# Optimization experiments

Measured on AMD Instinct MI355X. Metric: run time of the kernel, lower is better.

The kernel has to match this reference:

```python
import jax, jax.numpy as jnp
import numpy as np

NUM_HEADS = 16
EPS = 1e-5
CHUNK = 128  # chunk length for the chunked recurrent-state scan


def _linear_attention(x, Wq, Wk, Wv, Wo, bo):
    B, T, E = x.shape
    H = NUM_HEADS
    d = E // H

    def proj(W):
        # nn.Linear(bias=False): y = x @ W.T ; split heads -> (B,H,T,d)
        return (x @ W.T).reshape(B, T, H, d).transpose(0, 2, 1, 3)

    phi_q = jax.nn.elu(proj(Wq)) + 1.0
    phi_k = jax.nn.elu(proj(Wk)) + 1.0
    V = proj(Wv)

    nC = T // CHUNK
    # (nC, B, H, C, d) so lax.scan iterates over chunks of time
    def to_chunks(a):
        return a.reshape(B, H, nC, CHUNK, d).transpose(2, 0, 1, 3, 4)

    qc, kc, vc = to_chunks(phi_q), to_chunks(phi_k), to_chunks(V)
    mask = jnp.tril(jnp.ones((CHUNK, CHUNK), x.dtype))  # causal incl. diagonal

    S0 = jnp.zeros((B, H, d, d), x.dtype)  # running sum of k v^T
    z0 = jnp.zeros((B, H, d), x.dtype)     # running sum of phi_k

    def step(carry, inp):
        S, z = carry
        q, k, v = inp  # (B,H,C,d)
        A = jnp.einsum('bhid,bhjd->bhij', q, k) * mask
        num = jnp.einsum('bhij,bhjd->bhid', A, v) + jnp.einsum('bhid,bhde->bhie', q, S)
        den = jnp.sum(A, axis=-1) + jnp.einsum('bhid,bhd->bhi', q, z) + EPS
        out = num / den[..., None]
        S = S + jnp.einsum('bhjd,bhje->bhde', k, v)
        z = z + jnp.sum(k, axis=2)
        return (S, z), out

    _, outs = jax.lax.scan(step, (S0, z0), (qc, kc, vc))  # (nC,B,H,C,d)
    out = outs.transpose(1, 2, 0, 3, 4).reshape(B, H, T, d)
    out = out.transpose(0, 2, 1, 3).reshape(B, T, E)
    # out_proj (dropout p=0 / eval -> identity)
    return out @ Wo.T + bo


def setup_inputs() -> dict:
    key = jax.random.key(0)
    ks = jax.random.split(key, 6)
    B, T, E = 2, 2048, 1024
    s = 1.0 / np.sqrt(E)
    return {
        'x': jax.random.normal(ks[0], (B, T, E), jnp.float32),
        'Wq': jax.random.normal(ks[1], (E, E), jnp.float32) * s,
        'Wk': jax.random.normal(ks[2], (E, E), jnp.float32) * s,
        'Wv': jax.random.normal(ks[3], (E, E), jnp.float32) * s,
        'Wo': jax.random.normal(ks[4], (E, E), jnp.float32) * s,
        'bo': jnp.zeros((E,), jnp.float32),
    }


def reference(x, Wq, Wk, Wv, Wo, bo):
    return _linear_attention(x, Wq, Wk, Wv, Wo, bo)
```

## Files before the change

### kernel.cpp

```cpp
#include <hip/hip_runtime.h>
#include <hip/hip_bf16.h>
#include <stdint.h>

typedef __attribute__((ext_vector_type(4)))  float  floatx4;
typedef __attribute__((ext_vector_type(8)))  short  short8;
typedef __attribute__((ext_vector_type(8)))  unsigned short ushortx8;
typedef __attribute__((ext_vector_type(4)))  unsigned short ushortx4;

#define B_  2
#define T_  2048
#define E_  1024
#define H_  16
#define D_  64
#define C_  128
#define NC_ 16
#define M_  4096
#define EPS_ 1e-5f

__device__ __forceinline__ unsigned short f2b(float f) {
    union { float f; unsigned int u; } v; v.f = f;
    unsigned int r = v.u + 0x7fffu + ((v.u >> 16) & 1u);
    return (unsigned short)(r >> 16);
}
__device__ __forceinline__ float b2f(unsigned short b) {
    union { unsigned int u; float f; } v; v.u = ((unsigned int)b) << 16;
    return v.f;
}

__device__ __forceinline__ int stage_seg(int i) { return (i & 3) ^ ((i >> 3) & 3); }
__device__ __forceinline__ int frag_slot(int lane) {
    int m = lane & 15, q = lane >> 4;
    return m * 4 + (q ^ ((m >> 1) & 3));
}

__global__ __launch_bounds__(256) void convert_all(const float* __restrict__ x,
                                                   const float* __restrict__ Wq,
                                                   const float* __restrict__ Wk,
                                                   const float* __restrict__ Wv,
                                                   const float* __restrict__ Wo,
                                                   unsigned short* __restrict__ dst) {
    int i = (blockIdx.x * 256 + threadIdx.x) * 4;
    const float* s; int off;
    if (i < M_ * E_) { s = x; off = i; }
    else {
        int j = i - M_ * E_;
        int which = j >> 20;
        s = (which == 0) ? Wq : (which == 1) ? Wk : (which == 2) ? Wv : Wo;
        off = j & ((1 << 20) - 1);
    }
    float4 f = *(const float4*)(s + off);
    ushortx4 o;
    o[0] = f2b(f.x); o[1] = f2b(f.y); o[2] = f2b(f.z); o[3] = f2b(f.w);
    *(ushortx4*)(dst + i) = o;
}

__global__ __launch_bounds__(256) void gemm_qkv(const unsigned short* __restrict__ A,
                                                const unsigned short* __restrict__ Bm,
                                                unsigned short* __restrict__ Cb) {
    const int N = 3 * E_, K = E_;
    __shared__ __align__(16) unsigned short smem[32768];
    unsigned short* at0 = smem;
    unsigned short* bt0 = smem + 8192;
    unsigned short* at1 = smem + 16384;
    unsigned short* bt1 = smem + 24576;
    int tid = threadIdx.x;
    int wave = tid >> 6, lane = tid & 63;
    int wr = wave >> 1, wc = wave & 1;
    int m = lane & 15, q = lane >> 4;
    int srow = lane >> 2, sseg = stage_seg(lane);
    int fs = frag_slot(lane);
    int row0 = blockIdx.y * 128, col0 = blockIdx.x * 128;
    floatx4 acc[4][4];
    for (int i = 0; i < 4; i++) for (int j = 0; j < 4; j++) acc[i][j] = floatx4{0.f, 0.f, 0.f, 0.f};

    auto stage = [&](unsigned short* at, unsigned short* bt, int k0) {
        for (int p = 0; p < 4; p++) {
            int t = p * 4 + wave;
            const unsigned short* ga = A + (size_t)(row0 + (t & 7) * 16 + srow) * K + k0 + (t >> 3) * 32 + sseg * 8;
            __builtin_amdgcn_global_load_lds((const __attribute__((address_space(1))) unsigned int*)ga,
                (__attribute__((address_space(3))) unsigned int*)(at + t * 512), 16, 0, 0);
        }
        for (int p = 0; p < 4; p++) {
            int u = p * 4 + wave;
            const unsigned short* gb = Bm + (size_t)(col0 + (u & 7) * 16 + srow) * K + k0 + (u >> 3) * 32 + sseg * 8;
            __builtin_amdgcn_global_load_lds((const __attribute__((address_space(1))) unsigned int*)gb,
                (__attribute__((address_space(3))) unsigned int*)(bt + u * 512), 16, 0, 0);
        }
    };
    auto compute = [&](const unsigned short* at, const unsigned short* bt) {
        for (int kh = 0; kh < 2; kh++) {
            short8 af[4], bf[4];
            for (int mi = 0; mi < 4; mi++) af[mi] = *(const short8*)(at + (kh * 8 + wr * 4 + mi) * 512 + fs * 8);
            for (int ni = 0; ni < 4; ni++) bf[ni] = *(const short8*)(bt + (kh * 8 + wc * 4 + ni) * 512 + fs * 8);
            for (int mi = 0; mi < 4; mi++)
                for (int ni = 0; ni < 4; ni++)
                    acc[mi][ni] = __builtin_amdgcn_mfma_f32_16x16x32_bf16(af[mi], bf[ni], acc[mi][ni], 0, 0, 0);
        }
    };

    stage(at0, bt0, 0);
    __syncthreads();
    for (int k0 = 0; k0 < K; k0 += 128) {
        stage(at1, bt1, k0 + 64);
        compute(at0, bt0);
        __syncthreads();
        if (k0 + 128 < K) stage(at0, bt0, k0 + 128);
        compute(at1, bt1);
        __syncthreads();
    }

    unsigned short* epi = smem + wave * 2176;
    bool isphi = (col0 < 2 * E_);
    for (int half = 0; half < 2; half++) {
        if (half) asm volatile("" ::: "memory");
        for (int mi2 = 0; mi2 < 2; mi2++) {
            int mi = half * 2 + mi2;
            for (int ni = 0; ni < 4; ni++)
                for (int reg = 0; reg < 4; reg++) {
                    int lr = mi2 * 16 + q * 4 + reg;
                    float v = acc[mi][ni][reg];
                    if (isphi) v = (v > 0.f) ? (v + 1.f) : __expf(v);
                    epi[lr * 68 + ni * 16 + m] = f2b(v);
                }
        }
        for (int i = 0; i < 4; i++) {
            int s = i * 64 + lane;
            int lr = s >> 3, seg = s & 7;
            const unsigned short* p = epi + lr * 68 + seg * 8;
            ushortx4 lo = *(const ushortx4*)(p);
            ushortx4 hi = *(const ushortx4*)(p + 4);
            ushortx8 val;
            for (int e = 0; e < 4; e++) { val[e] = lo[e]; val[e + 4] = hi[e]; }
            int row = row0 + wr * 64 + half * 32 + lr;
            int col = col0 + wc * 64 + seg * 8;
            *(ushortx8*)(Cb + (size_t)row * N + col) = val;
        }
    }
}

__global__ __launch_bounds__(256) void gemm_out(const unsigned short* __restrict__ A,
                                                const unsigned short* __restrict__ Bm,
                                                const float* __restrict__ bias,
                                                float* __restrict__ Cf) {
    const int N = E_, K = E_;
    __shared__ __align__(16) unsigned short smem[24576];
    unsigned short* at0 = smem;
    unsigned short* bt0 = smem + 8192;
    unsigned short* at1 = smem + 12288;
    unsigned short* bt1 = smem + 20480;
    int tid = threadIdx.x;
    int wave = tid >> 6, lane = tid & 63;
    int wr = wave >> 1, wc = wave & 1;
    int m = lane & 15, q = lane >> 4;
    int srow = lane >> 2, sseg = stage_seg(lane);
    int fs = frag_slot(lane);
    int row0 = blockIdx.y * 128, col0 = blockIdx.x * 64;
    floatx4 acc[4][2];
    for (int i = 0; i < 4; i++) for (int j = 0; j < 2; j++) acc[i][j] = floatx4{0.f, 0.f, 0.f, 0.f};

    auto stage = [&](unsigned short* at, unsigned short* bt, int k0) {
        for (int p = 0; p < 4; p++) {
            int t = p * 4 + wave;
            const unsigned short* ga = A + (size_t)(row0 + (t & 7) * 16 + srow) * K + k0 + (t >> 3) * 32 + sseg * 8;
            __builtin_amdgcn_global_load_lds((const __attribute__((address_space(1))) unsigned int*)ga,
                (__attribute__((address_space(3))) unsigned int*)(at + t * 512), 16, 0, 0);
        }
        for (int p = 0; p < 2; p++) {
            int u = p * 4 + wave;
            const unsigned short* gb = Bm + (size_t)(col0 + (u & 3) * 16 + srow) * K + k0 + (u >> 2) * 32 + sseg * 8;
            __builtin_amdgcn_global_load_lds((const __attribute__((address_space(1))) unsigned int*)gb,
                (__attribute__((address_space(3))) unsigned int*)(bt + u * 512), 16, 0, 0);
        }
    };
    auto compute = [&](const unsigned short* at, const unsigned short* bt) {
        for (int kh = 0; kh < 2; kh++) {
            short8 af[4], bf[2];
            for (int mi = 0; mi < 4; mi++) af[mi] = *(const short8*)(at + (kh * 8 + wr * 4 + mi) * 512 + fs * 8);
            for (int ci = 0; ci < 2; ci++) bf[ci] = *(const short8*)(bt + (kh * 4 + wc * 2 + ci) * 512 + fs * 8);
            for (int mi = 0; mi < 4; mi++)
                for (int ci = 0; ci < 2; ci++)
                    acc[mi][ci] = __builtin_amdgcn_mfma_f32_16x16x32_bf16(af[mi], bf[ci], acc[mi][ci], 0, 0, 0);
        }
    };

    stage(at0, bt0, 0);
    __syncthreads();
    for (int k0 = 0; k0 < K; k0 += 128) {
        stage(at1, bt1, k0 + 64);
        compute(at0, bt0);
        __syncthreads();
        if (k0 + 128 < K) stage(at0, bt0, k0 + 128);
        compute(at1, bt1);
        __syncthreads();
    }

    int qrow = q * 4;
    for (int ci = 0; ci < 2; ci++) {
        int col = col0 + wc * 32 + ci * 16 + m;
        float bv = bias[col];
        for (int mi = 0; mi < 4; mi++)
            for (int r2 = 0; r2 < 4; r2++) {
                int row = row0 + wr * 64 + mi * 16 + qrow + r2;
                Cf[(size_t)row * N + col] = acc[mi][ci][r2] + bv;
            }
    }
}

__global__ __launch_bounds__(256) void chunk_sums(const unsigned short* __restrict__ qkv,
                                                  float* __restrict__ Sc, float* __restrict__ zc) {
    int c = blockIdx.x, h = blockIdx.y, bb = blockIdx.z;
    __shared__ __align__(16) unsigned short Kt[64 * 132];
    __shared__ __align__(16) unsigned short Vt[80 * 132];
    int tid = threadIdx.x;
    int lane = tid & 63, w = tid >> 6;
    size_t rowb = (size_t)bb * T_ + (size_t)c * C_;
    int kcol = E_ + h * D_, vcol = 2 * E_ + h * D_;

    {
        int r4 = (tid >> 3) * 4;
        int seg = (tid & 7) * 8;
        ushortx8 kv[4], vv[4];
        for (int t = 0; t < 4; t++) {
            size_t g = (rowb + r4 + t) * 3072;
            kv[t] = *(const ushortx8*)(qkv + g + kcol + seg);
            vv[t] = *(const ushortx8*)(qkv + g + vcol + seg);
        }
        for (int e = 0; e < 8; e++) {
            ushortx4 ka, va;
            for (int t = 0; t < 4; t++) { ka[t] = kv[t][e]; va[t] = vv[t][e]; }
            *(ushortx4*)(Kt + (seg + e) * 132 + r4) = ka;
            *(ushortx4*)(Vt + (seg + e) * 132 + r4) = va;
        }
    }
    if (tid < 128) Vt[64 * 132 + tid] = 0x3f80;
    __syncthreads();

    floatx4 acc[5];
    for (int ni = 0; ni < 5; ni++) acc[ni] = floatx4{0.f, 0.f, 0.f, 0.f};
    int lm = lane & 15, lk = (lane >> 4) * 8;
    for (int k0 = 0; k0 < 128; k0 += 32) {
        short8 af = *(const short8*)(Kt + (w * 16 + lm) * 132 + k0 + lk);
        for (int ni = 0; ni < 5; ni++) {
            short8 bf = *(const short8*)(Vt + (ni * 16 + lm) * 132 + k0 + lk);
            acc[ni] = __builtin_amdgcn_mfma_f32_16x16x32_bf16(af, bf, acc[ni], 0, 0, 0);
        }
    }
    size_t base = ((size_t)(bb * H_ + h) * NC_ + c) * (size_t)(D_ * D_);
    int r0 = w * 16 + (lane >> 4) * 4;
    for (int ni = 0; ni < 4; ni++)
        for (int reg = 0; reg < 4; reg++)
            Sc[base + (size_t)(r0 + reg) * D_ + ni * 16 + lm] = acc[ni][reg];
    if (lm == 0) {
        size_t zb = ((size_t)(bb * H_ + h) * NC_ + c) * D_;
        for (int reg = 0; reg < 4; reg++) zc[zb + r0 + reg] = acc[4][reg];
    }
}

__global__ __launch_bounds__(256) void attn_kernel(const unsigned short* __restrict__ qkv,
                                                   const float* __restrict__ Sc,
                                                   const float* __restrict__ zc,
                                                   unsigned short* __restrict__ attn) {
    int c = blockIdx.x, h = blockIdx.y, bb = blockIdx.z;
    __shared__ __align__(16) unsigned short qs[128 * 68];
    __shared__ __align__(16) unsigned short ks[128 * 68];
    __shared__ __align__(16) unsigned short vt[64 * 132];
    __shared__ __align__(16) unsigned short ovl[128 * 36];
    __shared__ float zsh[64];
    int tid = threadIdx.x;
    int lane = tid & 63, w = tid >> 6;
    int lm = lane & 15, lq = lane >> 4;
    size_t rowb = (size_t)bb * T_ + (size_t)c * C_;
    int qcol = h * D_, kcol = E_ + h * D_, vcol = 2 * E_ + h * D_;

    for (int s = 0; s < 4; s++) {
        int off = s * 256 + tid;
        int r = off >> 3, seg = (off & 7) * 8;
        size_t g = (rowb + r) * 3072;
        ushortx8 q8 = *(const ushortx8*)(qkv + g + qcol + seg);
        ushortx8 k8 = *(const ushortx8*)(qkv + g + kcol + seg);
        *(ushortx8*)(qs + r * 68 + seg) = q8;
        *(ushortx8*)(ks + r * 68 + seg) = k8;
    }
    {
        int r4 = (tid >> 3) * 4;
        int seg = (tid & 7) * 8;
        ushortx8 vv[4];
        for (int t = 0; t < 4; t++)
            vv[t] = *(const ushortx8*)(qkv + (rowb + r4 + t) * 3072 + vcol + seg);
        for (int e = 0; e < 8; e++) {
            ushortx4 va;
            for (int t = 0; t < 4; t++) va[t] = vv[t][e];
            *(ushortx4*)(vt + (seg + e) * 132 + r4) = va;
        }
    }
    {
        size_t scb = ((size_t)(bb * H_ + h) * NC_) * (size_t)(D_ * D_);
        int p = tid * 16;
        float a[16];
        for (int i = 0; i < 16; i++) a[i] = 0.f;
        for (int j = 0; j < c; j++) {
            const float* Sj = Sc + scb + (size_t)j * (D_ * D_) + p;
            for (int q = 0; q < 16; q += 4) {
                float4 f = *(const float4*)(Sj + q);
                a[q] += f.x; a[q + 1] += f.y; a[q + 2] += f.z; a[q + 3] += f.w;
            }
        }
        for (int i = 0; i < 16; i++) {
            int d = (p + i) >> 6, e = (p + i) & 63;
            ovl[e * 68 + d] = f2b(a[i]);
        }
    }
    if (tid < 64) {
        size_t zb = ((size_t)(bb * H_ + h) * NC_) * D_;
        float zr = 0.f;
        for (int j = 0; j < c; j++) zr += zc[zb + (size_t)j * D_ + tid];
        zsh[tid] = zr;
    }
    __syncthreads();

    floatx4 acc[2][4];
    for (int mi = 0; mi < 2; mi++) for (int ni = 0; ni < 4; ni++) acc[mi][ni] = floatx4{0.f, 0.f, 0.f, 0.f};
    for (int k0 = 0; k0 < 64; k0 += 32) {
        short8 aq[2];
        for (int mi = 0; mi < 2; mi++)
            aq[mi] = *(const short8*)(qs + (w * 32 + mi * 16 + lm) * 68 + k0 + lq * 8);
        for (int ni = 0; ni < 4; ni++) {
            short8 bs = *(const short8*)(ovl + (ni * 16 + lm) * 68 + k0 + lq * 8);
            for (int mi = 0; mi < 2; mi++)
                acc[mi][ni] = __builtin_amdgcn_mfma_f32_16x16x32_bf16(aq[mi], bs, acc[mi][ni], 0, 0, 0);
        }
    }
    float dsum[2][4];
    {
        int d0 = lm * 4;
        float4 z4 = *(const float4*)(zsh + d0);
        for (int mi = 0; mi < 2; mi++)
            for (int reg = 0; reg < 4; reg++) {
                int row = w * 32 + mi * 16 + lq * 4 + reg;
                ushortx4 q4 = *(const ushortx4*)(qs + row * 68 + d0);
                dsum[mi][reg] = b2f(q4[0]) * z4.x + b2f(q4[1]) * z4.y + b2f(q4[2]) * z4.z + b2f(q4[3]) * z4.w;
            }
    }
    __syncthreads();

    for (int jt = 0; jt <= w; jt++) {
        floatx4 pa[2][2];
        for (int mi = 0; mi < 2; mi++) for (int ct = 0; ct < 2; ct++) pa[mi][ct] = floatx4{0.f, 0.f, 0.f, 0.f};
        for (int k0 = 0; k0 < 64; k0 += 32) {
            short8 aq[2];
            for (int mi = 0; mi < 2; mi++)
                aq[mi] = *(const short8*)(qs + (w * 32 + mi * 16 + lm) * 68 + k0 + lq * 8);
            for (int ct = 0; ct < 2; ct++) {
                short8 bk = *(const short8*)(ks + (jt * 32 + ct * 16 + lm) * 68 + k0 + lq * 8);
                for (int mi = 0; mi < 2; mi++)
                    pa[mi][ct] = __builtin_amdgcn_mfma_f32_16x16x32_bf16(aq[mi], bk, pa[mi][ct], 0, 0, 0);
            }
        }
        bool diag = (jt == w);
        for (int mi = 0; mi < 2; mi++)
            for (int ct = 0; ct < 2; ct++)
                for (int reg = 0; reg < 4; reg++) {
                    int il = mi * 16 + lq * 4 + reg;
                    int jl = ct * 16 + lm;
                    float v = pa[mi][ct][reg];
                    if (diag && jl > il) v = 0.f;
                    dsum[mi][reg] += v;
                    ovl[(w * 32 + il) * 36 + jl] = f2b(v);
                }
        short8 ap[2];
        for (int mi = 0; mi < 2; mi++)
            ap[mi] = *(const short8*)(ovl + (w * 32 + mi * 16 + lm) * 36 + lq * 8);
        for (int ni = 0; ni < 4; ni++) {
            short8 bv = *(const short8*)(vt + (ni * 16 + lm) * 132 + jt * 32 + lq * 8);
            for (int mi = 0; mi < 2; mi++)
                acc[mi][ni] = __builtin_amdgcn_mfma_f32_16x16x32_bf16(ap[mi], bv, acc[mi][ni], 0, 0, 0);
        }
    }

    for (int off = 1; off < 16; off <<= 1)
        for (int mi = 0; mi < 2; mi++)
            for (int reg = 0; reg < 4; reg++)
                dsum[mi][reg] += __shfl_xor(dsum[mi][reg], off);

    for (int mi = 0; mi < 2; mi++)
        for (int reg = 0; reg < 4; reg++) {
            float inv = 1.f / (dsum[mi][reg] + EPS_);
            int row = w * 32 + mi * 16 + lq * 4 + reg;
            for (int ni = 0; ni < 4; ni++)
                attn[(rowb + row) * E_ + h * D_ + ni * 16 + lm] = f2b(acc[mi][ni][reg] * inv);
        }
}

extern "C" void kernel_launch(void* const* d_in, const int* in_sizes, int n_in,
                              void* d_out, int out_size, void* d_ws, size_t ws_size,
                              hipStream_t stream) {
    const float* x  = (const float*)d_in[0];
    const float* Wq = (const float*)d_in[1];
    const float* Wk = (const float*)d_in[2];
    const float* Wv = (const float*)d_in[3];
    const float* Wo = (const float*)d_in[4];
    const float* bo = (const float*)d_in[5];
    float* out = (float*)d_out;

    const size_t MB = 1024 * 1024;
    uint8_t* ws = (uint8_t*)d_ws;
    unsigned short* xb    = (unsigned short*)(ws + 0);
    unsigned short* wb    = (unsigned short*)(ws + 8 * MB);
    unsigned short* wob   = wb + 3 * E_ * E_;
    unsigned short* qkvb  = (unsigned short*)(ws + 16 * MB);
    float* Sc = (float*)(ws + 40 * MB);
    float* zc = (float*)(ws + 48 * MB);
    unsigned short* attnb = xb;

    convert_all<<<(M_ * E_ + 4 * E_ * E_) / 1024, 256, 0, stream>>>(x, Wq, Wk, Wv, Wo, xb);

    gemm_qkv<<<dim3(24, 32), 256, 0, stream>>>(xb, wb, qkvb);
    chunk_sums<<<dim3(NC_, H_, B_), 256, 0, stream>>>(qkvb, Sc, zc);
    attn_kernel<<<dim3(NC_, H_, B_), 256, 0, stream>>>(qkvb, Sc, zc, attnb);
    gemm_out<<<dim3(16, 32), 256, 0, stream>>>(attnb, wob, bo, out);
}
```

Baseline: 167.4 us.

## Split A/B staging and use fine-grained vmcnt waits in GEMM main loops

Both the QKV projection GEMM and the output projection GEMM now stage the A and B tiles separately. Full __syncthreads are replaced by raw s_barrier plus explicit s_waitcnt vmcnt counts, so only the loads for the tile about to be used must have landed. B-tile prefetches are issued between the two k-halves of MFMA work, and the MFMA bursts are wrapped in s_setprio to raise wave priority. The goal is more overlap of global-to-LDS traffic with matrix math and less barrier stall. The trade-off is that correctness now depends on hand-counted vmcnt values matching the exact number of loads each stage issues.

New measurement: 161.5 us. 1.04x faster.

```diff
diff --git a/kernel.cpp b/kernel.cpp
--- a/kernel.cpp
+++ b/kernel.cpp
@@ -73,13 +73,15 @@
     floatx4 acc[4][4];
     for (int i = 0; i < 4; i++) for (int j = 0; j < 4; j++) acc[i][j] = floatx4{0.f, 0.f, 0.f, 0.f};
 
-    auto stage = [&](unsigned short* at, unsigned short* bt, int k0) {
+    auto stageA = [&](unsigned short* at, int k0) {
         for (int p = 0; p < 4; p++) {
             int t = p * 4 + wave;
             const unsigned short* ga = A + (size_t)(row0 + (t & 7) * 16 + srow) * K + k0 + (t >> 3) * 32 + sseg * 8;
             __builtin_amdgcn_global_load_lds((const __attribute__((address_space(1))) unsigned int*)ga,
                 (__attribute__((address_space(3))) unsigned int*)(at + t * 512), 16, 0, 0);
         }
+    };
+    auto stageB = [&](unsigned short* bt, int k0) {
         for (int p = 0; p < 4; p++) {
             int u = p * 4 + wave;
             const unsigned short* gb = Bm + (size_t)(col0 + (u & 7) * 16 + srow) * K + k0 + (u >> 3) * 32 + sseg * 8;
@@ -87,26 +89,43 @@
                 (__attribute__((address_space(3))) unsigned int*)(bt + u * 512), 16, 0, 0);
         }
     };
-    auto compute = [&](const unsigned short* at, const unsigned short* bt) {
-        for (int kh = 0; kh < 2; kh++) {
-            short8 af[4], bf[4];
-            for (int mi = 0; mi < 4; mi++) af[mi] = *(const short8*)(at + (kh * 8 + wr * 4 + mi) * 512 + fs * 8);
-            for (int ni = 0; ni < 4; ni++) bf[ni] = *(const short8*)(bt + (kh * 8 + wc * 4 + ni) * 512 + fs * 8);
-            for (int mi = 0; mi < 4; mi++)
-                for (int ni = 0; ni < 4; ni++)
-                    acc[mi][ni] = __builtin_amdgcn_mfma_f32_16x16x32_bf16(af[mi], bf[ni], acc[mi][ni], 0, 0, 0);
-        }
-    };
-
-    stage(at0, bt0, 0);
-    __syncthreads();
+    short8 af[4], bf[4];
+    auto frags = [&](const unsigned short* at, const unsigned short* bt, int kh) {
+        for (int mi = 0; mi < 4; mi++) af[mi] = *(const short8*)(at + (kh * 8 + wr * 4 + mi) * 512 + fs * 8);
+        for (int ni = 0; ni < 4; ni++) bf[ni] = *(const short8*)(bt + (kh * 8 + wc * 4 + ni) * 512 + fs * 8);
+    };
+    auto mfma16 = [&]() {
+        __builtin_amdgcn_s_setprio(1);
+        for (int mi = 0; mi < 4; mi++)
+            for (int ni = 0; ni < 4; ni++)
+                acc[mi][ni] = __builtin_amdgcn_mfma_f32_16x16x32_bf16(af[mi], bf[ni], acc[mi][ni], 0, 0, 0);
+        __builtin_amdgcn_s_setprio(0);
+    };
+
+    stageA(at0, 0); stageB(bt0, 0);
     for (int k0 = 0; k0 < K; k0 += 128) {
-        stage(at1, bt1, k0 + 64);
-        compute(at0, bt0);
-        __syncthreads();
-        if (k0 + 128 < K) stage(at0, bt0, k0 + 128);
-        compute(at1, bt1);
-        __syncthreads();
+        stageA(at1, k0 + 64);
+        asm volatile("s_waitcnt vmcnt(4)" ::: "memory");
+        __builtin_amdgcn_s_barrier();
+        frags(at0, bt0, 0);
+        mfma16();
+        frags(at0, bt0, 1);
+        stageB(bt1, k0 + 64);
+        mfma16();
+        __builtin_amdgcn_s_barrier();
+        if (k0 + 128 < K) {
+            stageA(at0, k0 + 128);
+            asm volatile("s_waitcnt vmcnt(4)" ::: "memory");
+        } else {
+            asm volatile("s_waitcnt vmcnt(0)" ::: "memory");
+        }
+        __builtin_amdgcn_s_barrier();
+        frags(at1, bt1, 0);
+        mfma16();
+        frags(at1, bt1, 1);
+        if (k0 + 128 < K) stageB(bt0, k0 + 128);
+        mfma16();
+        __builtin_amdgcn_s_barrier();
     }
 
     unsigned short* epi = smem + wave * 2176;
@@ -158,13 +177,15 @@
     floatx4 acc[4][2];
     for (int i = 0; i < 4; i++) for (int j = 0; j < 2; j++) acc[i][j] = floatx4{0.f, 0.f, 0.f, 0.f};
 
-    auto stage = [&](unsigned short* at, unsigned short* bt, int k0) {
+    auto stageA = [&](unsigned short* at, int k0) {
         for (int p = 0; p < 4; p++) {
             int t = p * 4 + wave;
             const unsigned short* ga = A + (size_t)(row0 + (t & 7) * 16 + srow) * K + k0 + (t >> 3) * 32 + sseg * 8;
             __builtin_amdgcn_global_load_lds((const __attribute__((address_space(1))) unsigned int*)ga,
                 (__attribute__((address_space(3))) unsigned int*)(at + t * 512), 16, 0, 0);
         }
+    };
+    auto stageB = [&](unsigned short* bt, int k0) {
         for (int p = 0; p < 2; p++) {
             int u = p * 4 + wave;
             const unsigned short* gb = Bm + (size_t)(col0 + (u & 3) * 16 + srow) * K + k0 + (u >> 2) * 32 + sseg * 8;
@@ -172,26 +193,43 @@
                 (__attribute__((address_space(3))) unsigned int*)(bt + u * 512), 16, 0, 0);
         }
     };
-    auto compute = [&](const unsigned short* at, const unsigned short* bt) {
-        for (int kh = 0; kh < 2; kh++) {
-            short8 af[4], bf[2];
-            for (int mi = 0; mi < 4; mi++) af[mi] = *(const short8*)(at + (kh * 8 + wr * 4 + mi) * 512 + fs * 8);
-            for (int ci = 0; ci < 2; ci++) bf[ci] = *(const short8*)(bt + (kh * 4 + wc * 2 + ci) * 512 + fs * 8);
-            for (int mi = 0; mi < 4; mi++)
-                for (int ci = 0; ci < 2; ci++)
-                    acc[mi][ci] = __builtin_amdgcn_mfma_f32_16x16x32_bf16(af[mi], bf[ci], acc[mi][ci], 0, 0, 0);
-        }
-    };
-
-    stage(at0, bt0, 0);
-    __syncthreads();
+    short8 af[4], bf[2];
+    auto frags = [&](const unsigned short* at, const unsigned short* bt, int kh) {
+        for (int mi = 0; mi < 4; mi++) af[mi] = *(const short8*)(at + (kh * 8 + wr * 4 + mi) * 512 + fs * 8);
+        for (int ci = 0; ci < 2; ci++) bf[ci] = *(const short8*)(bt + (kh * 4 + wc * 2 + ci) * 512 + fs * 8);
+    };
+    auto mfma8 = [&]() {
+        __builtin_amdgcn_s_setprio(1);
+        for (int mi = 0; mi < 4; mi++)
+            for (int ci = 0; ci < 2; ci++)
+                acc[mi][ci] = __builtin_amdgcn_mfma_f32_16x16x32_bf16(af[mi], bf[ci], acc[mi][ci], 0, 0, 0);
+        __builtin_amdgcn_s_setprio(0);
+    };
+
+    stageA(at0, 0); stageB(bt0, 0);
     for (int k0 = 0; k0 < K; k0 += 128) {
-        stage(at1, bt1, k0 + 64);
-        compute(at0, bt0);
-        __syncthreads();
-        if (k0 + 128 < K) stage(at0, bt0, k0 + 128);
-        compute(at1, bt1);
-        __syncthreads();
+        stageA(at1, k0 + 64);
+        asm volatile("s_waitcnt vmcnt(4)" ::: "memory");
+        __builtin_amdgcn_s_barrier();
+        frags(at0, bt0, 0);
+        mfma8();
+        frags(at0, bt0, 1);
+        stageB(bt1, k0 + 64);
+        mfma8();
+        __builtin_amdgcn_s_barrier();
+        if (k0 + 128 < K) {
+            stageA(at0, k0 + 128);
+            asm volatile("s_waitcnt vmcnt(4)" ::: "memory");
+        } else {
+            asm volatile("s_waitcnt vmcnt(0)" ::: "memory");
+        }
+        __builtin_amdgcn_s_barrier();
+        frags(at1, bt1, 0);
+        mfma8();
+        frags(at1, bt1, 1);
+        if (k0 + 128 < K) stageB(bt0, k0 + 128);
+        mfma8();
+        __builtin_amdgcn_s_barrier();
     }
 
     int qrow = q * 4;
```
